# Kernel optimization log

Hardware: AMD Instinct MI355X
Metric: run time of the kernel (lower is better)

## Reference

```python
import jax, jax.numpy as jnp
from jax import lax
import numpy as np

B, S, T = 128, 256, 256
VOCAB, EMBED, ENC, DEC, DOF, LOOKBACK = 32000, 256, 256, 512, 4, 4


def setup_inputs() -> dict:
    key = jax.random.key(0)
    ks = jax.random.split(key, 20)
    w = lambda k, shape: jax.random.normal(k, shape, jnp.float32) * 0.05
    return {
        "in_seq": jax.random.randint(ks[0], (B, S), 0, VOCAB),
        "tgt_seq": jax.random.normal(ks[1], (B, T, DOF), jnp.float32),
        "lengths": jnp.full((B,), S, dtype=jnp.int32),
        "embedding": w(ks[2], (VOCAB, EMBED)),
        "enc_Wih_f": w(ks[3], (4 * ENC, EMBED)),
        "enc_Whh_f": w(ks[4], (4 * ENC, ENC)),
        "enc_b_f": w(ks[5], (4 * ENC,)),
        "enc_Wih_b": w(ks[6], (4 * ENC, EMBED)),
        "enc_Whh_b": w(ks[7], (4 * ENC, ENC)),
        "enc_b_b": w(ks[8], (4 * ENC,)),
        "dec_Wih": w(ks[9], (4 * DEC, DEC + LOOKBACK * DOF)),
        "dec_Whh": w(ks[10], (4 * DEC, DEC)),
        "dec_b": w(ks[11], (4 * DEC,)),
        "W_src": w(ks[12], (DEC, 2 * ENC)),
        "W_ctx": w(ks[13], (DEC, 2 * ENC + DEC)),
        "W_out": w(ks[14], (DOF, DEC)),
        "b_out": w(ks[15], (DOF,)),
    }


def _lstm_cell(x, h, c, Wih, Whh, b):
    # PyTorch gate order: i, f, g, o
    g = x @ Wih.T + h @ Whh.T + b
    i, f, gg, o = jnp.split(g, 4, axis=-1)
    c_new = jax.nn.sigmoid(f) * c + jax.nn.sigmoid(i) * jnp.tanh(gg)
    h_new = jax.nn.sigmoid(o) * jnp.tanh(c_new)
    return h_new, c_new


def _scan_lstm(xs, Wih, Whh, b, reverse=False):
    # xs: [T, B, E] -> hidden states [T, B, H] (aligned to original time order)
    Bsz, H = xs.shape[1], Whh.shape[1]
    h0 = jnp.zeros((Bsz, H), xs.dtype)

    def step(carry, x):
        h, c = carry
        h, c = _lstm_cell(x, h, c, Wih, Whh, b)
        return (h, c), h

    _, hs = lax.scan(step, (h0, h0), xs, reverse=reverse)
    return hs


def reference(in_seq, tgt_seq, lengths, embedding,
              enc_Wih_f, enc_Whh_f, enc_b_f,
              enc_Wih_b, enc_Whh_b, enc_b_b,
              dec_Wih, dec_Whh, dec_b,
              W_src, W_ctx, W_out, b_out):
    Bsz, Tlen = tgt_seq.shape[0], tgt_seq.shape[1]
    # ----- encoder (bi-LSTM, eval mode: dropout off, zero initial state) -----
    emb = embedding[in_seq]              # [B,S,E]
    xs = jnp.swapaxes(emb, 0, 1)         # [S,B,E]
    hf = _scan_lstm(xs, enc_Wih_f, enc_Whh_f, enc_b_f, reverse=False)
    hb = _scan_lstm(xs, enc_Wih_b, enc_Whh_b, enc_b_b, reverse=True)
    enc_out = jnp.swapaxes(jnp.concatenate([hf, hb], axis=-1), 0, 1)  # [B,S,2H]
    enc_mask = (in_seq == 0)             # [B,S]
    # precompute attention source projection once (same math as per-step)
    proj = jnp.einsum('bse,de->bsd', enc_out, W_src)  # [B,S,DEC]
    # ----- teacher-forced lookback windows of target frames -----
    pad = jnp.concatenate([jnp.zeros((Bsz, LOOKBACK, DOF), tgt_seq.dtype), tgt_seq], axis=1)
    win = jnp.stack([pad[:, k:k + Tlen] for k in range(LOOKBACK)], axis=2)  # [B,T,LB,DOF]
    win = win.reshape(Bsz, Tlen, LOOKBACK * DOF)
    win_t = jnp.swapaxes(win, 0, 1)      # [T,B,LB*DOF]
    h0 = jnp.zeros((Bsz, DEC), tgt_seq.dtype)

    def step(carry, w_t):
        h, c, feed = carry
        x = jnp.concatenate([w_t, feed], axis=-1)         # [B, LB*DOF + DEC]
        h, c = _lstm_cell(x, h, c, dec_Wih, dec_Whh, dec_b)
        scores = jnp.einsum('bd,bsd->bs', h, proj)        # Luong general score
        scores = jnp.where(enc_mask, -jnp.inf, scores)
        aw = jax.nn.softmax(scores, axis=-1)              # [B,S]
        ctx = jnp.einsum('bs,bse->be', aw, enc_out)       # [B,2H]
        feed = jnp.tanh(jnp.concatenate([h, ctx], axis=-1) @ W_ctx.T)
        out = feed @ W_out.T + b_out                      # [B,DOF]
        return (h, c, feed), (out, aw)

    _, (outs, aws) = lax.scan(step, (h0, h0, h0), win_t)
    dec_outputs = jnp.swapaxes(outs, 0, 1)   # [B,T,DOF]
    attn_weights = jnp.swapaxes(aws, 0, 1)   # [B,T,S]
    outputs = jnp.concatenate(
        [jnp.tanh(dec_outputs[..., :-1]), jax.nn.relu(dec_outputs[..., -1:])], axis=-1)
    return outputs, attn_weights
```

## Files before the change

kernel.cpp:

```cpp
#include <hip/hip_runtime.h>
#include <stdint.h>

#define B 128
#define S 256
#define T 256
#define EMBED 256
#define ENC 256
#define DEC 512
#define DOF 4

typedef __attribute__((ext_vector_type(8))) short bf16x8;
typedef __attribute__((ext_vector_type(4))) float f32x4;

static __device__ __forceinline__ float bf2f(unsigned short u){
  union{uint32_t u;float f;}c; c.u = ((uint32_t)u)<<16; return c.f;
}
static __device__ __forceinline__ unsigned short f2bf(float f){
  union{float f;uint32_t u;}c; c.f=f; uint32_t u=c.u;
  u += 0x7fffu + ((u>>16)&1u);
  return (unsigned short)(u>>16);
}
static __device__ __forceinline__ void unp2(uint32_t w, float&a, float&b){
  union{uint32_t u;float f;}c1,c2; c1.u = w<<16; c2.u = w & 0xffff0000u; a=c1.f; b=c2.f;
}
static __device__ __forceinline__ float sigm(float x){ return 1.0f/(1.0f+__expf(-x)); }

static __device__ __forceinline__ unsigned long long ldc8(const void* p){
  return __hip_atomic_load((unsigned long long*)p, __ATOMIC_RELAXED, __HIP_MEMORY_SCOPE_AGENT);
}
static __device__ __forceinline__ void stc8(void* p, unsigned long long v){
  __hip_atomic_store((unsigned long long*)p, v, __ATOMIC_RELAXED, __HIP_MEMORY_SCOPE_AGENT);
}
static __device__ __forceinline__ void stc4(void* p, unsigned v){
  __hip_atomic_store((unsigned*)p, v, __ATOMIC_RELAXED, __HIP_MEMORY_SCOPE_AGENT);
}
static __device__ __forceinline__ void stc4f(float* p, float v){
  __hip_atomic_store((unsigned*)p, __float_as_uint(v), __ATOMIC_RELAXED, __HIP_MEMORY_SCOPE_AGENT);
}
static __device__ __forceinline__ float ldc4f(const float* p){
  return __uint_as_float(__hip_atomic_load((const unsigned*)p, __ATOMIC_RELAXED, __HIP_MEMORY_SCOPE_AGENT));
}
union F16x8 { unsigned long long q[2]; bf16x8 v; unsigned short s[8]; };
union Ubf   { bf16x8 v; uint32_t u[4]; unsigned short s[8]; };
static __device__ __forceinline__ bf16x8 ldfrag_c(const unsigned short* p){
  F16x8 u; u.q[0] = ldc8(p); u.q[1] = ldc8(p + 4); return u.v;
}
static __device__ __forceinline__ unsigned long long pack4bf(float a,float b,float c,float d){
  return (unsigned long long)f2bf(a) | ((unsigned long long)f2bf(b)<<16)
       | ((unsigned long long)f2bf(c)<<32) | ((unsigned long long)f2bf(d)<<48);
}

#define CLINE 32
#define A_OFF 0
#define Q_OFF 16
#define C_OFF 32
#define F_OFF 48
#define PAIR_OFF 64
#define ENC_OFF 192
static __device__ __forceinline__ unsigned* cl(unsigned* c, int line){ return c + (size_t)line*CLINE; }

static __device__ __forceinline__ void bar_arr(unsigned* line){
  __builtin_amdgcn_s_waitcnt(0);
  __syncthreads();
  if (threadIdx.x == 0)
    __hip_atomic_fetch_add(line, 1u, __ATOMIC_RELAXED, __HIP_MEMORY_SCOPE_AGENT);
}
static __device__ __forceinline__ void barw(unsigned* set16, unsigned target){
  if (threadIdx.x < 64){
    unsigned* p = set16 + (size_t)(threadIdx.x & 15)*CLINE;
    while (!__all((int)(__hip_atomic_load(p, __ATOMIC_RELAXED, __HIP_MEMORY_SCOPE_AGENT) >= target)))
      __builtin_amdgcn_s_sleep(1);
  }
  __syncthreads();
  asm volatile("" ::: "memory");
}
static __device__ __forceinline__ void pair_sync(unsigned* line, unsigned target){
  __builtin_amdgcn_s_waitcnt(0);
  __syncthreads();
  if (threadIdx.x == 0){
    __hip_atomic_fetch_add(line, 1u, __ATOMIC_RELAXED, __HIP_MEMORY_SCOPE_AGENT);
    while (__hip_atomic_load(line, __ATOMIC_RELAXED, __HIP_MEMORY_SCOPE_AGENT) < target)
      __builtin_amdgcn_s_sleep(1);
  }
  __syncthreads();
  asm volatile("" ::: "memory");
}

static __device__ __forceinline__ int enc_idx(int s, int c){
  return s*256 + (((c & 24) | ((c ^ s) & 7)) << 3);
}

__global__ __launch_bounds__(256,1) void k_encoder(
  const unsigned short* __restrict__ emb,
  const unsigned short* __restrict__ WF, const unsigned short* __restrict__ WB,
  const float* __restrict__ bF, const float* __restrict__ bB,
  unsigned short* __restrict__ hEnc,
  unsigned short* __restrict__ encOut,
  unsigned* __restrict__ cntBase)
{
  __shared__ __align__(16) unsigned short Ws[16*520];
  __shared__ __align__(16) float Gs[64*17];
  __shared__ float bsh[16];
  const int bid = blockIdx.x;
  const int dir = bid >> 7;
  const int mg  = (bid >> 6) & 1;
  const int ng  = bid & 63;
  const int tid = threadIdx.x;
  const int lane = tid & 63, w = tid >> 6;
  const int l16 = lane & 15, qd = lane >> 4;
  const int m_base = mg * 64;
  unsigned* mycnt = cntBase + (size_t)dir*16*CLINE;
  unsigned* myline = cl(mycnt, bid & 15);

  const unsigned short* Wg = (dir ? WB : WF) + (size_t)ng*16*512;
  for (int i = tid; i < 16*64; i += 256){
    const int r = i >> 6, s = i & 63;
    *(uint4*)&Ws[r*520 + s*8] = *(const uint4*)&Wg[r*512 + s*8];
  }
  if (tid < 16) bsh[tid] = (dir ? bB : bF)[ng*16 + tid];
  float c[4] = {0.f,0.f,0.f,0.f};
  __syncthreads();

  for (int t = 0; t < S; ++t){
    const int tt = dir ? (S-1-t) : t;
    const unsigned short* Ae = emb + ((size_t)tt*B + m_base + w*16 + l16)*256 + qd*8;
    bf16x8 av[8];
#pragma unroll
    for (int ks = 0; ks < 8; ++ks) av[ks] = *(const bf16x8*)(Ae + ks*32);
    if (t) barw(mycnt, (unsigned)(8u*(unsigned)t));
    const unsigned short* Ah = hEnc + (((size_t)dir*2 + (size_t)(t&1))*B + m_base + w*16 + l16)*256 + qd*8;
    bf16x8 hf[8];
#pragma unroll
    for (int ks = 0; ks < 8; ++ks) hf[ks] = ldfrag_c(Ah + ks*32);
    f32x4 acc = (f32x4){0.f,0.f,0.f,0.f};
#pragma unroll
    for (int ks = 0; ks < 8; ++ks){
      bf16x8 bb = *(const bf16x8*)&Ws[l16*520 + ks*32 + qd*8];
      acc = __builtin_amdgcn_mfma_f32_16x16x32_bf16(av[ks], bb, acc, 0, 0, 0);
    }
#pragma unroll
    for (int ks = 0; ks < 8; ++ks){
      bf16x8 bb = *(const bf16x8*)&Ws[l16*520 + 256 + ks*32 + qd*8];
      acc = __builtin_amdgcn_mfma_f32_16x16x32_bf16(hf[ks], bb, acc, 0, 0, 0);
    }
    __syncthreads();
#pragma unroll
    for (int r = 0; r < 4; ++r)
      Gs[(w*16 + qd*4 + r)*17 + l16] = acc[r];
    __syncthreads();
    if (tid < 64){
      const int bl = tid;
      float hv[4];
#pragma unroll
      for (int u = 0; u < 4; ++u){
        const float gi = Gs[bl*17 + u*4 + 0] + bsh[u*4 + 0];
        const float gf = Gs[bl*17 + u*4 + 1] + bsh[u*4 + 1];
        const float gg = Gs[bl*17 + u*4 + 2] + bsh[u*4 + 2];
        const float go = Gs[bl*17 + u*4 + 3] + bsh[u*4 + 3];
        const float cn = sigm(gf)*c[u] + sigm(gi)*tanhf(gg);
        c[u] = cn;
        hv[u] = sigm(go)*tanhf(cn);
      }
      const int b2 = m_base + bl;
      const unsigned long long hq = pack4bf(hv[0],hv[1],hv[2],hv[3]);
      stc8(&hEnc[(((size_t)dir*2 + (size_t)((t+1)&1))*B + b2)*256 + ng*4], hq);
      *(unsigned long long*)&encOut[((size_t)b2*S + tt)*512 + dir*256 + ng*4] = hq;
    }
    bar_arr(myline);
  }
}

__global__ __launch_bounds__(256,2) void k_proj(
  const unsigned short* __restrict__ encOut,
  const unsigned short* __restrict__ WSP,
  unsigned short* __restrict__ proj)
{
  const int nb = blockIdx.x & 7;
  const int mt = blockIdx.x >> 3;
  const int tid = threadIdx.x;
  const int lane = tid & 63, w = tid >> 6;
  const int l16 = lane & 15, qd = lane >> 4;
  const int m0 = mt*64 + w*16;
  const unsigned short* Ap = encOut + ((size_t)m0 + l16)*512 + qd*8;
  bf16x8 av[16];
#pragma unroll
  for (int ks = 0; ks < 16; ++ks) av[ks] = *(const bf16x8*)(Ap + ks*32);
  for (int nn = 0; nn < 4; ++nn){
    const int qn = nb*4 + nn;
    const unsigned short* Bq = WSP + (size_t)qn*16*512 + (size_t)lane*8;
    f32x4 acc = (f32x4){0.f,0.f,0.f,0.f};
#pragma unroll
    for (int ks = 0; ks < 16; ++ks){
      bf16x8 bb = *(const bf16x8*)(Bq + (size_t)ks*512);
      acc = __builtin_amdgcn_mfma_f32_16x16x32_bf16(av[ks], bb, acc, 0, 0, 0);
    }
    const int d = qn*16 + l16, dh = d >> 8, dl = d & 255;
#pragma unroll
    for (int r = 0; r < 4; ++r){
      const int m = m0 + qd*4 + r;
      const int bb2 = m >> 8, s = m & 255;
      proj[(((size_t)bb2*2 + dh)*256 + s)*256 + dl] = f2bf(acc[r]);
    }
  }
}

__global__ __launch_bounds__(256,1) void k_decoder(
  const unsigned short* __restrict__ win,
  const unsigned short* __restrict__ WDx,
  const float* __restrict__ bD,
  const unsigned short* __restrict__ WCx,
  const unsigned short* __restrict__ projq,
  const unsigned short* __restrict__ encOut,
  const int* __restrict__ in_seq,
  const float* __restrict__ Wout, const float* __restrict__ bout,
  unsigned short* __restrict__ hdec,
  unsigned short* __restrict__ feed,
  unsigned short* __restrict__ ctxb,
  float* __restrict__ scp,
  float* __restrict__ out_main, float* __restrict__ out_attn,
  unsigned* __restrict__ cnts)
{
  __shared__ __align__(16) unsigned short encS[65536];
  __shared__ __align__(16) float scrf[1600];
  __shared__ float bsh[16];
  const int bid = blockIdx.x;
  const int b  = bid >> 1, eh = bid & 1;
  const int mg = bid & 1, ng = (bid >> 1) & 127;
  const int tid = threadIdx.x;
  const int lane = tid & 63, w = tid >> 6;
  const int l16 = lane & 15, qd = lane >> 4;
  const int m_base = mg*64;

  if (tid < 16) bsh[tid] = bD[ng*16 + tid];
  const int mymask = (in_seq[b*S + tid] == 0);
  {
    const unsigned short* Pq = projq + (((size_t)b*2 + eh)*256)*256;
    for (int i = 0; i < 32; ++i){
      const int s = i*8 + (tid>>5), cc = tid & 31;
      const uint4 v = *(const uint4*)&Pq[(size_t)s*256 + cc*8];
      *(uint4*)&encS[enc_idx(s, cc)] = v;
    }
  }
  float c[4] = {0.f,0.f,0.f,0.f};
  __syncthreads();

  for (int t = 0; t < T; ++t){
    const int row = m_base + w*16 + l16;
    const unsigned short* Aw = win  + ((size_t)t*B + row)*64 + qd*8;
    const unsigned short* Af = feed + (size_t)row*512 + qd*8;
    const unsigned short* Ah = hdec + ((size_t)(t&1)*B + row)*512 + qd*8;
    const unsigned short* Bp = WDx + (size_t)ng*34*512 + (size_t)lane*8;
    f32x4 acc = (f32x4){0.f,0.f,0.f,0.f};
    {
      bf16x8 hv[16];
#pragma unroll
      for (int i = 0; i < 16; ++i) hv[i] = ldfrag_c(Ah + i*32);
#pragma unroll
      for (int ks = 0; ks < 16; ++ks){
        bf16x8 bb = *(const bf16x8*)(Bp + (size_t)(18+ks)*512);
        acc = __builtin_amdgcn_mfma_f32_16x16x32_bf16(hv[ks], bb, acc, 0, 0, 0);
      }
    }
    bf16x8 bv0[18];
#pragma unroll
    for (int ks = 0; ks < 18; ++ks) bv0[ks] = *(const bf16x8*)(Bp + (size_t)ks*512);
    bf16x8 a0 = *(const bf16x8*)(Aw);
    bf16x8 a1 = *(const bf16x8*)(Aw + 32);
    if (t) barw(cl(cnts, F_OFF), (unsigned)(4u*(unsigned)t));
    {
      bf16x8 av[18];
      av[0] = a0; av[1] = a1;
#pragma unroll
      for (int i = 0; i < 16; ++i) av[2+i] = ldfrag_c(Af + i*32);
#pragma unroll
      for (int ks = 0; ks < 18; ++ks)
        acc = __builtin_amdgcn_mfma_f32_16x16x32_bf16(av[ks], bv0[ks], acc, 0, 0, 0);
    }
    __syncthreads();
#pragma unroll
    for (int r = 0; r < 4; ++r)
      scrf[(w*16 + qd*4 + r)*17 + l16] = acc[r];
    __syncthreads();
    if (tid < 64){
      float hv[4];
#pragma unroll
      for (int u = 0; u < 4; ++u){
        const float gi = scrf[tid*17 + u*4 + 0] + bsh[u*4 + 0];
        const float gf = scrf[tid*17 + u*4 + 1] + bsh[u*4 + 1];
        const float gg = scrf[tid*17 + u*4 + 2] + bsh[u*4 + 2];
        const float go = scrf[tid*17 + u*4 + 3] + bsh[u*4 + 3];
        const float cn = sigm(gf)*c[u] + sigm(gi)*tanhf(gg);
        c[u] = cn;
        hv[u] = sigm(go)*tanhf(cn);
      }
      stc8(&hdec[((size_t)((t+1)&1)*B + m_base + tid)*512 + ng*4],
           pack4bf(hv[0],hv[1],hv[2],hv[3]));
    }
    bar_arr(cl(cnts, A_OFF + (bid & 15)));

    if ((bid & 1) && t > 0){
      const int b2o = bid >> 1;
      const int d = tid >> 6, kk = lane;
      const unsigned short* fp = feed + (size_t)b2o*512 + kk*8;
      F16x8 u; u.q[0] = ldc8(fp); u.q[1] = ldc8(fp + 4);
      const float* wp = Wout + d*512 + kk*8;
      float p = 0.f;
#pragma unroll
      for (int j2 = 0; j2 < 8; ++j2) p += bf2f(u.s[j2]) * wp[j2];
#pragma unroll
      for (int off = 32; off > 0; off >>= 1) p += __shfl_down(p, off, 64);
      if (kk == 0){
        const float v = p + bout[d];
        out_main[((size_t)b2o*T + (t-1))*4 + d] = (d < 3) ? tanhf(v) : fmaxf(v, 0.f);
      }
    }

    barw(cl(cnts, A_OFF), (unsigned)(16u*(unsigned)(t+1)));
    if (tid < 64){
      F16x8 uq; uq.q[0] = ldc8(hdec + ((size_t)((t+1)&1)*B + b)*512 + eh*256 + tid*4);
      scrf[tid*4+0] = bf2f(uq.s[0]); scrf[tid*4+1] = bf2f(uq.s[1]);
      scrf[tid*4+2] = bf2f(uq.s[2]); scrf[tid*4+3] = bf2f(uq.s[3]);
    }
    __syncthreads();
    float sc = 0.f;
#pragma unroll 8
    for (int cix = 0; cix < 32; ++cix){
      Ubf u8; u8.v = *(const bf16x8*)&encS[enc_idx(tid, cix)];
      float f0,f1,f2,f3,f4,f5,f6,f7;
      unp2(u8.u[0],f0,f1); unp2(u8.u[1],f2,f3); unp2(u8.u[2],f4,f5); unp2(u8.u[3],f6,f7);
      const float* qp = &scrf[cix*8];
      sc += f0*qp[0] + f1*qp[1] + f2*qp[2] + f3*qp[3]
          + f4*qp[4] + f5*qp[5] + f6*qp[6] + f7*qp[7];
    }
    stc4f(&scp[((size_t)b*2 + eh)*256 + tid], sc);
    pair_sync(cl(cnts, PAIR_OFF + b), (unsigned)(2u*(unsigned)(t+1)));
    float tot = sc + ldc4f(&scp[((size_t)b*2 + (1-eh))*256 + tid]);
    if (mymask) tot = -1e30f;
    float mx = tot;
#pragma unroll
    for (int off = 32; off > 0; off >>= 1) mx = fmaxf(mx, __shfl_xor(mx, off, 64));
    if (lane == 0) scrf[512 + w] = mx;
    __syncthreads();
    mx = fmaxf(fmaxf(scrf[512], scrf[513]), fmaxf(scrf[514], scrf[515]));
    const float e = __expf(tot - mx);
    float l = e;
#pragma unroll
    for (int off = 32; off > 0; off >>= 1) l += __shfl_xor(l, off, 64);
    if (lane == 0) scrf[516 + w] = l;
    __syncthreads();
    l = scrf[516] + scrf[517] + scrf[518] + scrf[519];
    const float aw = e / l;
    scrf[256 + tid] = aw;
    if (eh == 0) __builtin_nontemporal_store(aw, &out_attn[((size_t)b*T + t)*S + tid]);
    __syncthreads();
    {
      float a[8] = {0,0,0,0,0,0,0,0};
      const int cc = lane & 31, par = lane >> 5;
      const unsigned short* Ep = encOut + ((size_t)b*S)*512 + eh*256 + cc*8;
#pragma unroll 8
      for (int i2 = 0; i2 < 32; ++i2){
        const int srow = w*64 + i2*2 + par;
        const float wgt = scrf[256 + srow];
        Ubf u8; u8.v = *(const bf16x8*)(Ep + (size_t)srow*512);
        float f0,f1,f2,f3,f4,f5,f6,f7;
        unp2(u8.u[0],f0,f1); unp2(u8.u[1],f2,f3); unp2(u8.u[2],f4,f5); unp2(u8.u[3],f6,f7);
        a[0]+=wgt*f0; a[1]+=wgt*f1; a[2]+=wgt*f2; a[3]+=wgt*f3;
        a[4]+=wgt*f4; a[5]+=wgt*f5; a[6]+=wgt*f6; a[7]+=wgt*f7;
      }
#pragma unroll
      for (int j2 = 0; j2 < 8; ++j2) a[j2] += __shfl_xor(a[j2], 32, 64);
      if (par == 0){
#pragma unroll
        for (int j2 = 0; j2 < 8; ++j2) scrf[528 + w*256 + cc*8 + j2] = a[j2];
      }
    }
    __syncthreads();
    if (tid < 128){
      const int e2 = tid*2;
      const float s0 = scrf[528+e2]     + scrf[528+256+e2]     + scrf[528+512+e2]     + scrf[528+768+e2];
      const float s1 = scrf[528+e2+1]   + scrf[528+256+e2+1]   + scrf[528+512+e2+1]   + scrf[528+768+e2+1];
      stc4(&ctxb[(size_t)b*512 + eh*256 + e2],
           (unsigned)f2bf(s0) | ((unsigned)f2bf(s1) << 16));
    }
    bar_arr(cl(cnts, C_OFF + (bid & 15)));

    if ((bid & 3) == 3){
      const int fblk = bid >> 2, fm = fblk >> 5, fn = fblk & 31;
      const int frow = fm*64 + w*16 + l16;
      const unsigned short* Fh = hdec + ((size_t)((t+1)&1)*B + frow)*512 + qd*8;
      const unsigned short* Fc = ctxb + (size_t)frow*512 + qd*8;
      const unsigned short* Bf = WCx + (size_t)fn*32*512 + (size_t)lane*8;
      f32x4 fa = (f32x4){0.f,0.f,0.f,0.f};
      {
        bf16x8 av[16];
#pragma unroll
        for (int ks = 0; ks < 16; ++ks) av[ks] = ldfrag_c(Fh + ks*32);
#pragma unroll
        for (int ks = 0; ks < 16; ++ks){
          bf16x8 bb = *(const bf16x8*)(Bf + (size_t)ks*512);
          fa = __builtin_amdgcn_mfma_f32_16x16x32_bf16(av[ks], bb, fa, 0, 0, 0);
        }
      }
      bf16x8 bv2[16];
#pragma unroll
      for (int ks = 0; ks < 16; ++ks) bv2[ks] = *(const bf16x8*)(Bf + (size_t)(16+ks)*512);
      barw(cl(cnts, C_OFF), (unsigned)(16u*(unsigned)(t+1)));
      {
        bf16x8 av[16];
#pragma unroll
        for (int ks = 0; ks < 16; ++ks) av[ks] = ldfrag_c(Fc + ks*32);
#pragma unroll
        for (int ks = 0; ks < 16; ++ks)
          fa = __builtin_amdgcn_mfma_f32_16x16x32_bf16(av[ks], bv2[ks], fa, 0, 0, 0);
      }
      __syncthreads();
#pragma unroll
      for (int r = 0; r < 4; ++r)
        scrf[(w*16 + qd*4 + r)*17 + l16] = tanhf(fa[r]);
      __syncthreads();
      if (tid < 64){
        const int fb = fm*64 + tid;
#pragma unroll
        for (int u = 0; u < 4; ++u)
          stc8(&feed[(size_t)fb*512 + fn*16 + u*4],
               pack4bf(scrf[tid*17+u*4+0], scrf[tid*17+u*4+1],
                       scrf[tid*17+u*4+2], scrf[tid*17+u*4+3]));
      }
      bar_arr(cl(cnts, F_OFF + ((bid >> 2) & 15)));
    }
  }
  if (bid & 1){
    barw(cl(cnts, F_OFF), (unsigned)(4u*256u));
    const int b2o = bid >> 1;
    const int d = tid >> 6, kk = lane;
    const unsigned short* fp = feed + (size_t)b2o*512 + kk*8;
    F16x8 u; u.q[0] = ldc8(fp); u.q[1] = ldc8(fp + 4);
    const float* wp = Wout + d*512 + kk*8;
    float p = 0.f;
#pragma unroll
    for (int j2 = 0; j2 < 8; ++j2) p += bf2f(u.s[j2]) * wp[j2];
#pragma unroll
    for (int off = 32; off > 0; off >>= 1) p += __shfl_down(p, off, 64);
    if (kk == 0){
      const float v = p + bout[d];
      out_main[((size_t)b2o*T + 255)*4 + d] = (d < 3) ? tanhf(v) : fmaxf(v, 0.f);
    }
  }
}

__global__ __launch_bounds__(256) void k_build_encw(
  const float* __restrict__ WihF, const float* __restrict__ WhhF,
  const float* __restrict__ WihB, const float* __restrict__ WhhB,
  unsigned short* WF, unsigned short* WB)
{
  const int idx = blockIdx.x*256 + threadIdx.x;
  const int dir = idx >> 19;
  const int i2 = idx & 524287;
  const int row = i2 >> 9, col = i2 & 511;
  const int j = row >> 2, g = row & 3;
  const int orig = g*256 + j;
  const float* Wih = dir ? WihB : WihF;
  const float* Whh = dir ? WhhB : WhhF;
  const float v = (col < 256) ? Wih[orig*256 + col] : Whh[orig*256 + (col-256)];
  (dir ? WB : WF)[i2] = f2bf(v);
}

__global__ __launch_bounds__(256) void k_build_decw(
  const float* __restrict__ Wih, const float* __restrict__ Whh, unsigned short* WDx)
{
  const int idx = blockIdx.x*256 + threadIdx.x;
  if (idx >= 2048*1088) return;
  const int row = idx / 1088, col = idx - row*1088;
  const int j = row >> 2, g = row & 3;
  const int orig = g*512 + j;
  float v;
  if (col < 16)        v = Wih[orig*528 + col];
  else if (col < 64)   v = 0.f;
  else if (col < 576)  v = Wih[orig*528 + (col - 48)];
  else                 v = Whh[orig*512 + (col - 576)];
  const int ng = row >> 4, l16 = row & 15;
  const int ks = col >> 5, qdd = (col >> 3) & 3, jj = col & 7;
  WDx[(((size_t)ng*34 + ks)*64 + qdd*16 + l16)*8 + jj] = f2bf(v);
}

__global__ __launch_bounds__(256) void k_build_wcx(
  const float* __restrict__ Wctx, unsigned short* WCx)
{
  const int idx = blockIdx.x*256 + threadIdx.x;
  const int n = idx >> 10, k = idx & 1023;
  const int fn = n >> 4, l16 = n & 15;
  const int ks = k >> 5, qdd = (k >> 3) & 3, jj = k & 7;
  WCx[(((size_t)fn*32 + ks)*64 + qdd*16 + l16)*8 + jj] = f2bf(Wctx[(size_t)n*1024 + k]);
}

__global__ __launch_bounds__(256) void k_build_wsp(
  const float* __restrict__ Wsrc, unsigned short* WSP)
{
  const int idx = blockIdx.x*256 + threadIdx.x;
  const int d = idx >> 9, e = idx & 511;
  const int qn = d >> 4, l16 = d & 15;
  const int ks = e >> 5, qdd = (e >> 3) & 3, jj = e & 7;
  WSP[(((size_t)qn*16 + ks)*64 + qdd*16 + l16)*8 + jj] = f2bf(Wsrc[(size_t)d*512 + e]);
}

__global__ __launch_bounds__(256) void k_build_bias(
  const float* __restrict__ ebF, const float* __restrict__ ebB,
  const float* __restrict__ dB, float* bF, float* bB, float* bD)
{
  const int idx = blockIdx.x*256 + threadIdx.x;
  if (idx < 1024) bF[idx] = ebF[(idx&3)*256 + (idx>>2)];
  else if (idx < 2048){ const int i = idx-1024; bB[i] = ebB[(i&3)*256 + (i>>2)]; }
  else { const int i = idx-2048; bD[i] = dB[(i&3)*512 + (i>>2)]; }
}

__global__ __launch_bounds__(256) void k_embed(
  const int* __restrict__ in_seq, const float* __restrict__ table, unsigned short* emb)
{
  const int idx = blockIdx.x*256 + threadIdx.x;
  const int e = idx & 255, b = (idx >> 8) & 127, s = idx >> 15;
  const int tok = in_seq[b*S + s];
  emb[idx] = f2bf(table[(size_t)tok*256 + e]);
}

__global__ __launch_bounds__(256) void k_win(
  const float* __restrict__ tgt, unsigned short* win)
{
  const int idx = blockIdx.x*256 + threadIdx.x;
  const int c = idx & 63, b = (idx >> 6) & 127, t = idx >> 13;
  float v = 0.f;
  if (c < 16){
    const int k = c >> 2, jj = c & 3;
    const int ts = t + k - 4;
    if (ts >= 0) v = tgt[((size_t)b*T + ts)*4 + jj];
  }
  win[idx] = f2bf(v);
}

extern "C" void kernel_launch(void* const* d_in, const int* in_sizes, int n_in,
                              void* d_out, int out_size, void* d_ws, size_t ws_size,
                              hipStream_t stream)
{
  const int*   in_seq    = (const int*)d_in[0];
  const float* tgt       = (const float*)d_in[1];
  const float* embedding = (const float*)d_in[3];
  const float* eWihF = (const float*)d_in[4];
  const float* eWhhF = (const float*)d_in[5];
  const float* ebF   = (const float*)d_in[6];
  const float* eWihB = (const float*)d_in[7];
  const float* eWhhB = (const float*)d_in[8];
  const float* ebB   = (const float*)d_in[9];
  const float* dWih  = (const float*)d_in[10];
  const float* dWhh  = (const float*)d_in[11];
  const float* dB    = (const float*)d_in[12];
  const float* Wsrc  = (const float*)d_in[13];
  const float* Wctx  = (const float*)d_in[14];
  const float* Wout  = (const float*)d_in[15];
  const float* bout  = (const float*)d_in[16];

  char* ws = (char*)d_ws;
  size_t off = 0;
  auto al = [&](size_t bytes)->char*{
    char* p = ws + off; off += (bytes + 255) & ~(size_t)255; return p; };

  char* stateBase = ws;
  unsigned short* hEnc = (unsigned short*)al(262144);
  unsigned short* hdec = (unsigned short*)al(262144);
  unsigned short* feed = (unsigned short*)al(131072);
  unsigned short* ctxb = (unsigned short*)al(131072);
  unsigned*       cnts = (unsigned*)al(28672);
  const size_t stateBytes = off;

  unsigned short* emb    = (unsigned short*)al(16777216);
  unsigned short* win    = (unsigned short*)al(4194304);
  unsigned short* encOut = (unsigned short*)al(33554432);
  unsigned short* proj   = (unsigned short*)al(33554432);
  unsigned short* WF     = (unsigned short*)al(1048576);
  unsigned short* WB     = (unsigned short*)al(1048576);
  unsigned short* WDx    = (unsigned short*)al(4456448);
  unsigned short* WCx    = (unsigned short*)al(1048576);
  unsigned short* WSP    = (unsigned short*)al(524288);
  float*          scp    = (float*)al(262144);
  float* bFr = (float*)al(4096);
  float* bBr = (float*)al(4096);
  float* bDr = (float*)al(8192);
  (void)ws_size; (void)in_sizes; (void)n_in; (void)out_size;

  float* out_main = (float*)d_out;
  float* out_attn = out_main + (size_t)B*T*DOF;

  const dim3 blk(256);
  k_build_encw <<<4096,  blk, 0, stream>>>(eWihF, eWhhF, eWihB, eWhhB, WF, WB);
  k_build_decw <<<8704,  blk, 0, stream>>>(dWih, dWhh, WDx);
  k_build_wcx  <<<2048,  blk, 0, stream>>>(Wctx, WCx);
  k_build_wsp  <<<1024,  blk, 0, stream>>>(Wsrc, WSP);
  k_build_bias <<<16,    blk, 0, stream>>>(ebF, ebB, dB, bFr, bBr, bDr);
  k_embed      <<<32768, blk, 0, stream>>>(in_seq, embedding, emb);
  k_win        <<<8192,  blk, 0, stream>>>(tgt, win);
  hipMemsetAsync(stateBase, 0, stateBytes, stream);

  k_encoder<<<256, blk, 0, stream>>>(emb, WF, WB, bFr, bBr, hEnc, encOut,
                                     cnts + (size_t)ENC_OFF*CLINE);

  k_proj<<<4096, blk, 0, stream>>>(encOut, WSP, proj);

  k_decoder<<<256, blk, 0, stream>>>(win, WDx, bDr, WCx, proj, encOut, in_seq,
                                     Wout, bout, hdec, feed, ctxb, scp,
                                     out_main, out_attn, cnts);
}
```

Measured before the change: 10.12 ms.

## Split attention over sequence halves with flash-style softmax merge, removing pair sync

Each block pair now splits attention along the source sequence (128 positions each) rather than the projection dimension. Each block computes a local max, sum and unnormalised partial context and publishes them. The fused feed GEMM merges the two halves with online-softmax rescaling when it loads the context. This removes the per-step pair barrier that used to sit between score computation and softmax, moving the wait off the critical path to the attention-weight write. In exchange it stores fp32 partial contexts, which doubles that traffic, and adds exp work in the feed stage.

```diff
diff --git a/kernel.cpp b/kernel.cpp
--- a/kernel.cpp
+++ b/kernel.cpp
@@ -31,17 +31,10 @@
 static __device__ __forceinline__ void stc8(void* p, unsigned long long v){
   __hip_atomic_store((unsigned long long*)p, v, __ATOMIC_RELAXED, __HIP_MEMORY_SCOPE_AGENT);
 }
-static __device__ __forceinline__ void stc4(void* p, unsigned v){
-  __hip_atomic_store((unsigned*)p, v, __ATOMIC_RELAXED, __HIP_MEMORY_SCOPE_AGENT);
-}
-static __device__ __forceinline__ void stc4f(float* p, float v){
-  __hip_atomic_store((unsigned*)p, __float_as_uint(v), __ATOMIC_RELAXED, __HIP_MEMORY_SCOPE_AGENT);
-}
-static __device__ __forceinline__ float ldc4f(const float* p){
-  return __uint_as_float(__hip_atomic_load((const unsigned*)p, __ATOMIC_RELAXED, __HIP_MEMORY_SCOPE_AGENT));
-}
 union F16x8 { unsigned long long q[2]; bf16x8 v; unsigned short s[8]; };
 union Ubf   { bf16x8 v; uint32_t u[4]; unsigned short s[8]; };
+union F32x2 { unsigned long long q; float f[2]; };
+union F32x8c{ unsigned long long q[4]; float f[8]; };
 static __device__ __forceinline__ bf16x8 ldfrag_c(const unsigned short* p){
   F16x8 u; u.q[0] = ldc8(p); u.q[1] = ldc8(p + 4); return u.v;
 }
@@ -52,7 +45,6 @@
 
 #define CLINE 32
 #define A_OFF 0
-#define Q_OFF 16
 #define C_OFF 32
 #define F_OFF 48
 #define PAIR_OFF 64
@@ -74,20 +66,9 @@
   __syncthreads();
   asm volatile("" ::: "memory");
 }
-static __device__ __forceinline__ void pair_sync(unsigned* line, unsigned target){
-  __builtin_amdgcn_s_waitcnt(0);
-  __syncthreads();
-  if (threadIdx.x == 0){
-    __hip_atomic_fetch_add(line, 1u, __ATOMIC_RELAXED, __HIP_MEMORY_SCOPE_AGENT);
-    while (__hip_atomic_load(line, __ATOMIC_RELAXED, __HIP_MEMORY_SCOPE_AGENT) < target)
-      __builtin_amdgcn_s_sleep(1);
-  }
-  __syncthreads();
-  asm volatile("" ::: "memory");
-}
-
-static __device__ __forceinline__ int enc_idx(int s, int c){
-  return s*256 + (((c & 24) | ((c ^ s) & 7)) << 3);
+
+static __device__ __forceinline__ int lds_off(int s, int g){
+  return s*512 + (((g & 56) | ((g ^ s) & 7)) << 3);
 }
 
 __global__ __launch_bounds__(256,1) void k_encoder(
@@ -194,12 +175,12 @@
       bf16x8 bb = *(const bf16x8*)(Bq + (size_t)ks*512);
       acc = __builtin_amdgcn_mfma_f32_16x16x32_bf16(av[ks], bb, acc, 0, 0, 0);
     }
-    const int d = qn*16 + l16, dh = d >> 8, dl = d & 255;
+    const int d = qn*16 + l16;
 #pragma unroll
     for (int r = 0; r < 4; ++r){
       const int m = m0 + qd*4 + r;
       const int bb2 = m >> 8, s = m & 255;
-      proj[(((size_t)bb2*2 + dh)*256 + s)*256 + dl] = f2bf(acc[r]);
+      proj[(((size_t)bb2*2 + (s >> 7))*128 + (s & 127))*512 + d] = f2bf(acc[r]);
     }
   }
 }
@@ -215,30 +196,32 @@
   const float* __restrict__ Wout, const float* __restrict__ bout,
   unsigned short* __restrict__ hdec,
   unsigned short* __restrict__ feed,
-  unsigned short* __restrict__ ctxb,
-  float* __restrict__ scp,
+  float* __restrict__ ctxp,
+  float* __restrict__ mlp,
   float* __restrict__ out_main, float* __restrict__ out_attn,
   unsigned* __restrict__ cnts)
 {
   __shared__ __align__(16) unsigned short encS[65536];
-  __shared__ __align__(16) float scrf[1600];
+  __shared__ __align__(16) float scrf[3296];
   __shared__ float bsh[16];
   const int bid = blockIdx.x;
-  const int b  = bid >> 1, eh = bid & 1;
+  const int b  = bid >> 1, sh = bid & 1;
   const int mg = bid & 1, ng = (bid >> 1) & 127;
   const int tid = threadIdx.x;
   const int lane = tid & 63, w = tid >> 6;
   const int l16 = lane & 15, qd = lane >> 4;
   const int m_base = mg*64;
+  const int r = tid >> 1;
 
   if (tid < 16) bsh[tid] = bD[ng*16 + tid];
-  const int mymask = (in_seq[b*S + tid] == 0);
+  const int mymask = (in_seq[b*S + sh*128 + r] == 0);
   {
-    const unsigned short* Pq = projq + (((size_t)b*2 + eh)*256)*256;
+    const unsigned short* Pq = projq + (((size_t)b*2 + sh)*128)*512;
     for (int i = 0; i < 32; ++i){
-      const int s = i*8 + (tid>>5), cc = tid & 31;
-      const uint4 v = *(const uint4*)&Pq[(size_t)s*256 + cc*8];
-      *(uint4*)&encS[enc_idx(s, cc)] = v;
+      const int gid = i*256 + tid;
+      const int s = gid >> 6, g = gid & 63;
+      const uint4 v = *(const uint4*)&Pq[(size_t)s*512 + g*8];
+      *(uint4*)&encS[lds_off(s, g)] = v;
     }
   }
   float c[4] = {0.f,0.f,0.f,0.f};
@@ -278,8 +261,8 @@
     }
     __syncthreads();
 #pragma unroll
-    for (int r = 0; r < 4; ++r)
-      scrf[(w*16 + qd*4 + r)*17 + l16] = acc[r];
+    for (int rr = 0; rr < 4; ++rr)
+      scrf[(w*16 + qd*4 + rr)*17 + l16] = acc[rr];
     __syncthreads();
     if (tid < 64){
       float hv[4];
@@ -317,78 +300,77 @@
 
     barw(cl(cnts, A_OFF), (unsigned)(16u*(unsigned)(t+1)));
     if (tid < 64){
-      F16x8 uq; uq.q[0] = ldc8(hdec + ((size_t)((t+1)&1)*B + b)*512 + eh*256 + tid*4);
-      scrf[tid*4+0] = bf2f(uq.s[0]); scrf[tid*4+1] = bf2f(uq.s[1]);
-      scrf[tid*4+2] = bf2f(uq.s[2]); scrf[tid*4+3] = bf2f(uq.s[3]);
+      F16x8 uh; const unsigned short* hp = hdec + ((size_t)((t+1)&1)*B + b)*512 + tid*8;
+      uh.q[0] = ldc8(hp); uh.q[1] = ldc8(hp + 4);
+#pragma unroll
+      for (int j = 0; j < 8; ++j) scrf[tid*8 + j] = bf2f(uh.s[j]);
     }
     __syncthreads();
     float sc = 0.f;
+    {
+      const int dh = tid & 1;
 #pragma unroll 8
-    for (int cix = 0; cix < 32; ++cix){
-      Ubf u8; u8.v = *(const bf16x8*)&encS[enc_idx(tid, cix)];
-      float f0,f1,f2,f3,f4,f5,f6,f7;
-      unp2(u8.u[0],f0,f1); unp2(u8.u[1],f2,f3); unp2(u8.u[2],f4,f5); unp2(u8.u[3],f6,f7);
-      const float* qp = &scrf[cix*8];
-      sc += f0*qp[0] + f1*qp[1] + f2*qp[2] + f3*qp[3]
-          + f4*qp[4] + f5*qp[5] + f6*qp[6] + f7*qp[7];
-    }
-    stc4f(&scp[((size_t)b*2 + eh)*256 + tid], sc);
-    pair_sync(cl(cnts, PAIR_OFF + b), (unsigned)(2u*(unsigned)(t+1)));
-    float tot = sc + ldc4f(&scp[((size_t)b*2 + (1-eh))*256 + tid]);
-    if (mymask) tot = -1e30f;
-    float mx = tot;
+      for (int cix = 0; cix < 32; ++cix){
+        const int g = dh*32 + cix;
+        Ubf u8; u8.v = *(const bf16x8*)&encS[lds_off(r, g)];
+        float f0,f1,f2,f3,f4,f5,f6,f7;
+        unp2(u8.u[0],f0,f1); unp2(u8.u[1],f2,f3); unp2(u8.u[2],f4,f5); unp2(u8.u[3],f6,f7);
+        const float* qp = &scrf[dh*256 + cix*8];
+        sc += f0*qp[0] + f1*qp[1] + f2*qp[2] + f3*qp[3]
+            + f4*qp[4] + f5*qp[5] + f6*qp[6] + f7*qp[7];
+      }
+    }
+    sc += __shfl_xor(sc, 1, 64);
+    if (mymask) sc = -1e30f;
+    float mx = sc;
 #pragma unroll
     for (int off = 32; off > 0; off >>= 1) mx = fmaxf(mx, __shfl_xor(mx, off, 64));
-    if (lane == 0) scrf[512 + w] = mx;
-    __syncthreads();
-    mx = fmaxf(fmaxf(scrf[512], scrf[513]), fmaxf(scrf[514], scrf[515]));
-    const float e = __expf(tot - mx);
-    float l = e;
-#pragma unroll
-    for (int off = 32; off > 0; off >>= 1) l += __shfl_xor(l, off, 64);
-    if (lane == 0) scrf[516 + w] = l;
-    __syncthreads();
-    l = scrf[516] + scrf[517] + scrf[518] + scrf[519];
-    const float aw = e / l;
-    scrf[256 + tid] = aw;
-    if (eh == 0) __builtin_nontemporal_store(aw, &out_attn[((size_t)b*T + t)*S + tid]);
-    __syncthreads();
+    if (lane == 0) scrf[1100 + w] = mx;
+    __syncthreads();
+    mx = fmaxf(fmaxf(scrf[1100], scrf[1101]), fmaxf(scrf[1102], scrf[1103]));
+    const float ee = __expf(sc - mx);
+    if (!(tid & 1)) scrf[1120 + r] = ee;
+    float lsum = (tid & 1) ? 0.f : ee;
+#pragma unroll
+    for (int off = 32; off > 0; off >>= 1) lsum += __shfl_xor(lsum, off, 64);
+    if (lane == 0) scrf[1104 + w] = lsum;
+    __syncthreads();
+    lsum = scrf[1104] + scrf[1105] + scrf[1106] + scrf[1107];
+    if (tid == 0){
+      F32x2 u; u.f[0] = mx; u.f[1] = lsum;
+      stc8(&mlp[((size_t)b*2 + sh)*2], u.q);
+    }
     {
       float a[8] = {0,0,0,0,0,0,0,0};
-      const int cc = lane & 31, par = lane >> 5;
-      const unsigned short* Ep = encOut + ((size_t)b*S)*512 + eh*256 + cc*8;
+      const unsigned short* Ep = encOut + ((size_t)(b*S + sh*128 + w*32))*512 + lane*8;
 #pragma unroll 8
       for (int i2 = 0; i2 < 32; ++i2){
-        const int srow = w*64 + i2*2 + par;
-        const float wgt = scrf[256 + srow];
-        Ubf u8; u8.v = *(const bf16x8*)(Ep + (size_t)srow*512);
+        const float wgt = scrf[1120 + w*32 + i2];
+        Ubf u8; u8.v = *(const bf16x8*)(Ep + (size_t)i2*512);
         float f0,f1,f2,f3,f4,f5,f6,f7;
         unp2(u8.u[0],f0,f1); unp2(u8.u[1],f2,f3); unp2(u8.u[2],f4,f5); unp2(u8.u[3],f6,f7);
         a[0]+=wgt*f0; a[1]+=wgt*f1; a[2]+=wgt*f2; a[3]+=wgt*f3;
         a[4]+=wgt*f4; a[5]+=wgt*f5; a[6]+=wgt*f6; a[7]+=wgt*f7;
       }
 #pragma unroll
-      for (int j2 = 0; j2 < 8; ++j2) a[j2] += __shfl_xor(a[j2], 32, 64);
-      if (par == 0){
-#pragma unroll
-        for (int j2 = 0; j2 < 8; ++j2) scrf[528 + w*256 + cc*8 + j2] = a[j2];
-      }
-    }
-    __syncthreads();
-    if (tid < 128){
+      for (int j2 = 0; j2 < 8; ++j2) scrf[1248 + w*512 + lane*8 + j2] = a[j2];
+    }
+    __syncthreads();
+    {
       const int e2 = tid*2;
-      const float s0 = scrf[528+e2]     + scrf[528+256+e2]     + scrf[528+512+e2]     + scrf[528+768+e2];
-      const float s1 = scrf[528+e2+1]   + scrf[528+256+e2+1]   + scrf[528+512+e2+1]   + scrf[528+768+e2+1];
-      stc4(&ctxb[(size_t)b*512 + eh*256 + e2],
-           (unsigned)f2bf(s0) | ((unsigned)f2bf(s1) << 16));
+      const float s0 = scrf[1248+e2]   + scrf[1248+512+e2]   + scrf[1248+1024+e2]   + scrf[1248+1536+e2];
+      const float s1 = scrf[1248+e2+1] + scrf[1248+512+e2+1] + scrf[1248+1024+e2+1] + scrf[1248+1536+e2+1];
+      F32x2 u; u.f[0] = s0; u.f[1] = s1;
+      stc8(&ctxp[((size_t)b*2 + sh)*512 + e2], u.q);
     }
     bar_arr(cl(cnts, C_OFF + (bid & 15)));
+    if (tid == 0)
+      __hip_atomic_fetch_add(cl(cnts, PAIR_OFF + b), 1u, __ATOMIC_RELAXED, __HIP_MEMORY_SCOPE_AGENT);
 
     if ((bid & 3) == 3){
       const int fblk = bid >> 2, fm = fblk >> 5, fn = fblk & 31;
       const int frow = fm*64 + w*16 + l16;
       const unsigned short* Fh = hdec + ((size_t)((t+1)&1)*B + frow)*512 + qd*8;
-      const unsigned short* Fc = ctxb + (size_t)frow*512 + qd*8;
       const unsigned short* Bf = WCx + (size_t)fn*32*512 + (size_t)lane*8;
       f32x4 fa = (f32x4){0.f,0.f,0.f,0.f};
       {
@@ -405,18 +387,30 @@
 #pragma unroll
       for (int ks = 0; ks < 16; ++ks) bv2[ks] = *(const bf16x8*)(Bf + (size_t)(16+ks)*512);
       barw(cl(cnts, C_OFF), (unsigned)(16u*(unsigned)(t+1)));
-      {
-        bf16x8 av[16];
-#pragma unroll
-        for (int ks = 0; ks < 16; ++ks) av[ks] = ldfrag_c(Fc + ks*32);
-#pragma unroll
-        for (int ks = 0; ks < 16; ++ks)
-          fa = __builtin_amdgcn_mfma_f32_16x16x32_bf16(av[ks], bv2[ks], fa, 0, 0, 0);
+      F32x2 u0, u1;
+      u0.q = ldc8(&mlp[((size_t)frow*2 + 0)*2]);
+      u1.q = ldc8(&mlp[((size_t)frow*2 + 1)*2]);
+      const float M  = fmaxf(u0.f[0], u1.f[0]);
+      const float a0 = __expf(u0.f[0] - M), a1 = __expf(u1.f[0] - M);
+      const float Lr = u0.f[1]*a0 + u1.f[1]*a1;
+      const float w0 = a0/Lr, w1 = a1/Lr;
+#pragma unroll
+      for (int ks = 0; ks < 16; ++ks){
+        const int kk = ks*32 + qd*8;
+        const float* p0 = &ctxp[((size_t)frow*2 + 0)*512 + kk];
+        const float* p1 = &ctxp[((size_t)frow*2 + 1)*512 + kk];
+        F32x8c c0, c1;
+        c0.q[0]=ldc8(p0); c0.q[1]=ldc8(p0+2); c0.q[2]=ldc8(p0+4); c0.q[3]=ldc8(p0+6);
+        c1.q[0]=ldc8(p1); c1.q[1]=ldc8(p1+2); c1.q[2]=ldc8(p1+4); c1.q[3]=ldc8(p1+6);
+        Ubf o;
+#pragma unroll
+        for (int j2 = 0; j2 < 8; ++j2) o.s[j2] = f2bf(w0*c0.f[j2] + w1*c1.f[j2]);
+        fa = __builtin_amdgcn_mfma_f32_16x16x32_bf16(o.v, bv2[ks], fa, 0, 0, 0);
       }
       __syncthreads();
 #pragma unroll
-      for (int r = 0; r < 4; ++r)
-        scrf[(w*16 + qd*4 + r)*17 + l16] = tanhf(fa[r]);
+      for (int rr = 0; rr < 4; ++rr)
+        scrf[(w*16 + qd*4 + rr)*17 + l16] = tanhf(fa[rr]);
       __syncthreads();
       if (tid < 64){
         const int fb = fm*64 + tid;
@@ -427,6 +421,29 @@
                        scrf[tid*17+u*4+2], scrf[tid*17+u*4+3]));
       }
       bar_arr(cl(cnts, F_OFF + ((bid >> 2) & 15)));
+      {
+        F32x2 up; up.q = ldc8(&mlp[((size_t)b*2 + (1-sh))*2]);
+        const float M2 = fmaxf(mx, up.f[0]);
+        const float L2 = lsum*__expf(mx - M2) + up.f[1]*__expf(up.f[0] - M2);
+        const float scale = __expf(mx - M2)/L2;
+        if (!(tid & 1))
+          __builtin_nontemporal_store(scrf[1120 + r]*scale,
+                                      &out_attn[((size_t)b*T + t)*S + sh*128 + r]);
+      }
+    } else {
+      if (tid == 0){
+        unsigned* pp = cl(cnts, PAIR_OFF + b);
+        while (__hip_atomic_load(pp, __ATOMIC_RELAXED, __HIP_MEMORY_SCOPE_AGENT) < 2u*(unsigned)(t+1))
+          __builtin_amdgcn_s_sleep(1);
+      }
+      __syncthreads();
+      F32x2 up; up.q = ldc8(&mlp[((size_t)b*2 + (1-sh))*2]);
+      const float M2 = fmaxf(mx, up.f[0]);
+      const float L2 = lsum*__expf(mx - M2) + up.f[1]*__expf(up.f[0] - M2);
+      const float scale = __expf(mx - M2)/L2;
+      if (!(tid & 1))
+        __builtin_nontemporal_store(scrf[1120 + r]*scale,
+                                    &out_attn[((size_t)b*T + t)*S + sh*128 + r]);
     }
   }
   if (bid & 1){
@@ -566,7 +583,6 @@
   unsigned short* hEnc = (unsigned short*)al(262144);
   unsigned short* hdec = (unsigned short*)al(262144);
   unsigned short* feed = (unsigned short*)al(131072);
-  unsigned short* ctxb = (unsigned short*)al(131072);
   unsigned*       cnts = (unsigned*)al(28672);
   const size_t stateBytes = off;
 
@@ -579,7 +595,8 @@
   unsigned short* WDx    = (unsigned short*)al(4456448);
   unsigned short* WCx    = (unsigned short*)al(1048576);
   unsigned short* WSP    = (unsigned short*)al(524288);
-  float*          scp    = (float*)al(262144);
+  float*          ctxp   = (float*)al(524288);
+  float*          mlp    = (float*)al(2048);
   float* bFr = (float*)al(4096);
   float* bBr = (float*)al(4096);
   float* bDr = (float*)al(8192);
@@ -604,6 +621,6 @@
   k_proj<<<4096, blk, 0, stream>>>(encOut, WSP, proj);
 
   k_decoder<<<256, blk, 0, stream>>>(win, WDx, bDr, WCx, proj, encOut, in_seq,
-                                     Wout, bout, hdec, feed, ctxb, scp,
+                                     Wout, bout, hdec, feed, ctxp, mlp,
                                      out_main, out_attn, cnts);
 }
```

Measured after the change: 12.48 ms. 1.23x slower.
